# Kernel optimization log

Hardware: AMD Instinct MI355X
Metric: run time of the kernel (lower is better)

## Reference

```python
import jax, jax.numpy as jnp
import numpy as np

B, C_IN, C_OUT, H, W = 4, 256, 256, 64, 64
KH = KW = 3
STRIDE = 1
PAD = 1
DIL = 1


def setup_inputs() -> dict:
    key = jax.random.key(0)
    k1, k2, k3, k4 = jax.random.split(key, 4)
    x = jax.random.normal(k1, (B, C_IN, H, W), dtype=jnp.float32)
    # torchvision layout: 2*dg*KH*KW channels, (y, x) pair per kernel tap
    offset = jax.random.normal(k2, (B, 2 * KH * KW, H, W), dtype=jnp.float32)
    fan_in = C_IN * KH * KW
    weight = jax.random.normal(k3, (C_OUT, C_IN, KH, KW), dtype=jnp.float32) / np.sqrt(fan_in)
    bias = jax.random.normal(k4, (C_OUT,), dtype=jnp.float32) * 0.01
    return {"x": x, "offset": offset, "weight": weight, "bias": bias}


def _gather_bilinear_corner(x_flat, yi, xi, h, w):
    # x_flat: [B, C, H*W]; yi/xi: [B, KK, Ho, Wo] int32
    valid = ((yi >= 0) & (yi < h) & (xi >= 0) & (xi < w)).astype(x_flat.dtype)
    idx = jnp.clip(yi, 0, h - 1) * w + jnp.clip(xi, 0, w - 1)
    b = idx.shape[0]
    g = jnp.take_along_axis(x_flat, idx.reshape(b, 1, -1), axis=2)
    return g.reshape(b, x_flat.shape[1], *yi.shape[1:]), valid


def deform_conv2d(x, offset, weight, bias):
    b, c, h, w = x.shape
    o = weight.shape[0]
    kk = KH * KW
    ho = (h + 2 * PAD - DIL * (KH - 1) - 1) // STRIDE + 1
    wo = (w + 2 * PAD - DIL * (KW - 1) - 1) // STRIDE + 1

    ky = (jnp.arange(kk, dtype=jnp.float32) // KW) * DIL  # [KK]
    kx = (jnp.arange(kk, dtype=jnp.float32) % KW) * DIL
    hs = jnp.arange(ho, dtype=jnp.float32) * STRIDE - PAD   # [Ho]
    ws = jnp.arange(wo, dtype=jnp.float32) * STRIDE - PAD   # [Wo]

    off = offset.reshape(b, kk, 2, ho, wo)
    py = hs[None, None, :, None] + ky[None, :, None, None] + off[:, :, 0]  # [B,KK,Ho,Wo]
    px = ws[None, None, None, :] + kx[None, :, None, None] + off[:, :, 1]

    y0 = jnp.floor(py)
    x0 = jnp.floor(px)
    wy1 = py - y0  # fractional parts, differentiable w.r.t. offsets
    wx1 = px - x0
    wy0 = 1.0 - wy1
    wx0 = 1.0 - wx1
    y0i = y0.astype(jnp.int32)
    x0i = x0.astype(jnp.int32)

    x_flat = x.reshape(b, c, h * w)
    corners = [
        (y0i,     x0i,     wy0 * wx0),
        (y0i,     x0i + 1, wy0 * wx1),
        (y0i + 1, x0i,     wy1 * wx0),
        (y0i + 1, x0i + 1, wy1 * wx1),
    ]
    sampled = jnp.zeros((b, c, kk, ho, wo), dtype=x.dtype)
    for yi, xi, wgt in corners:
        g, valid = _gather_bilinear_corner(x_flat, yi, xi, h, w)
        sampled = sampled + g * (wgt * valid)[:, None]

    out = jnp.einsum('bckhw,ock->bohw', sampled, weight.reshape(o, c, kk))
    return out + bias[None, :, None, None]


def reference(x, offset, weight, bias):
    return deform_conv2d(x, offset, weight, bias)
```

## Files before the change

kernel.cpp:

```cpp
#include <hip/hip_runtime.h>

typedef __bf16 bf16;
typedef __bf16 bf16x4 __attribute__((ext_vector_type(4)));
typedef __bf16 bf16x8 __attribute__((ext_vector_type(8)));
typedef float  f32x4  __attribute__((ext_vector_type(4)));
typedef float  f32x16 __attribute__((ext_vector_type(16)));
typedef unsigned int u32x4 __attribute__((ext_vector_type(4)));

#define KK     9
#define KDIM   2304
#define KSTEPS 144
#define PXW    64

__device__ __forceinline__ int sreadi(int v) {
    return __builtin_amdgcn_readfirstlane(v);
}

__device__ __forceinline__ float BL(unsigned v) {
    return __builtin_bit_cast(float, v << 16);
}
__device__ __forceinline__ float BH(unsigned v) {
    return __builtin_bit_cast(float, v & 0xffff0000u);
}

__global__ __launch_bounds__(256) void prep2_k(const float* __restrict__ x,
                                               const float* __restrict__ w,
                                               bf16* __restrict__ xt,
                                               bf16* __restrict__ wq) {
    __shared__ __align__(16) char smem[8 * 2308 * 2];
    int bid = blockIdx.x;
    int tid = threadIdx.x;
    if (bid < 1024) {
        float (*tileF)[65] = reinterpret_cast<float(*)[65]>(smem);
        int pt = bid & 63, ct = (bid >> 6) & 3, b = bid >> 8;
        const float* src = x + ((size_t)(b * 256 + ct * 64)) * 4096 + pt * 64;
        int f4 = tid & 15;
        int cl = tid >> 4;
        #pragma unroll
        for (int q = 0; q < 4; ++q) {
            int c = q * 16 + cl;
            f32x4 v = *reinterpret_cast<const f32x4*>(src + (size_t)c * 4096 + f4 * 4);
            tileF[f4 * 4 + 0][c] = v[0];
            tileF[f4 * 4 + 1][c] = v[1];
            tileF[f4 * 4 + 2][c] = v[2];
            tileF[f4 * 4 + 3][c] = v[3];
        }
        __syncthreads();
        int j = tid & 7, p0 = tid >> 3;
        bf16* dst = xt + ((size_t)(b * 4096 + pt * 64)) * 256 + ct * 64 + j * 8;
        #pragma unroll
        for (int pp = 0; pp < 2; ++pp) {
            int p = p0 + pp * 32;
            bf16x8 sv;
            #pragma unroll
            for (int k = 0; k < 8; ++k) sv[k] = (bf16)tileF[p][j * 8 + k];
            *reinterpret_cast<bf16x8*>(dst + (size_t)p * 256) = sv;
        }
    } else {
        bf16 (*Wl)[2308] = reinterpret_cast<bf16(*)[2308]>(smem);
        int wb     = bid - 1024;
        int o_base = wb * 8;
        int m      = o_base >> 5;
        int o31b   = o_base & 31;
        #pragma unroll
        for (int pass = 0; pass < 18; ++pass) {
            int i    = pass * 256 + tid;
            int r    = i / 576;
            int col4 = i - r * 576;
            f32x4 v = *reinterpret_cast<const f32x4*>(
                w + (size_t)(o_base + r) * KDIM + col4 * 4);
            Wl[r][col4 * 4 + 0] = (bf16)v[0];
            Wl[r][col4 * 4 + 1] = (bf16)v[1];
            Wl[r][col4 * 4 + 2] = (bf16)v[2];
            Wl[r][col4 * 4 + 3] = (bf16)v[3];
        }
        __syncthreads();
        #pragma unroll
        for (int pass = 0; pass < 9; ++pass) {
            int gid  = pass * 256 + tid;
            int ol   = gid & 7;
            int half = (gid >> 3) & 1;
            int ks   = gid >> 4;
            int kb   = ks * 16 + half * 8;
            int tap  = kb >> 8;
            int cc0  = kb & 255;
            bf16x8 sv;
            #pragma unroll
            for (int j = 0; j < 8; ++j) sv[j] = Wl[ol][(cc0 + j) * 9 + tap];
            size_t g = (size_t)((m * KSTEPS + ks) * 64 + half * 32 + o31b + ol);
            *reinterpret_cast<bf16x8*>(wq + g * 8) = sv;
        }
    }
}

__global__ __launch_bounds__(1024, 4) void deform_gemm_k(
    const bf16*  __restrict__ xt,
    const float* __restrict__ off,
    const bf16*  __restrict__ wq,
    const float* __restrict__ bias,
    float*       __restrict__ out) {

    __shared__ bf16 S[2][PXW * 256];

    int tid   = threadIdx.x;
    int wavei = sreadi(tid >> 6);
    int lane  = tid & 63;
    int l32   = lane & 31;
    int half  = lane >> 5;
    int mt    = wavei & 7;
    int kh    = wavei >> 3;

    int bid   = blockIdx.x;
    int pb    = ((bid & 7) << 5) | (bid >> 3);
    int pix0  = pb * PXW;
    int b     = pix0 >> 12;
    int pimgb = pix0 & 4095;
    int obase = b * 73728;
    int rot   = (bid >> 3) & 7;

    int n0    = wavei * 4 + half * 2;
    int n1    = n0 + 1;
    int pimg0 = pimgb + n0;
    int pimg1 = pimgb + n1;
    const char* xb = (const char*)xt + ((size_t)b << 21) + l32 * 16;

    f32x16 acc0, acc1;
    #pragma unroll
    for (int r = 0; r < 16; ++r) { acc0[r] = 0.f; acc1[r] = 0.f; }

    auto body = [&](int n, int pimg, float oy, float ox, int ty, int tx,
                    bf16* Sw) {
        float py = (float)((pimg >> 6) + ty) + oy;
        float px = (float)((pimg & 63) + tx) + ox;
        float fy = floorf(py), fx = floorf(px);
        int   y0 = (int)fy,    x0 = (int)fx;
        float wy1 = py - fy, wx1 = px - fx;
        float wy0 = 1.f - wy1, wx0 = 1.f - wx1;
        wy0 = ((unsigned)y0       < 64u) ? wy0 : 0.f;
        wy1 = ((unsigned)(y0 + 1) < 64u) ? wy1 : 0.f;
        wx0 = ((unsigned)x0       < 64u) ? wx0 : 0.f;
        wx1 = ((unsigned)(x0 + 1) < 64u) ? wx1 : 0.f;
        int yc0 = min(max(y0, 0), 63), yc1 = min(max(y0 + 1, 0), 63);
        int xc0 = min(max(x0, 0), 63), xc1 = min(max(x0 + 1, 0), 63);
        unsigned u0 = (unsigned)(yc0 * 64 + xc0) * 512u;
        unsigned u1 = (unsigned)(yc0 * 64 + xc1) * 512u;
        unsigned u2 = (unsigned)(yc1 * 64 + xc0) * 512u;
        unsigned u3 = (unsigned)(yc1 * 64 + xc1) * 512u;
        float w0 = wy0 * wx0, w1 = wy0 * wx1;
        float w2 = wy1 * wx0, w3 = wy1 * wx1;
        u32x4 g0 = *(const u32x4*)(xb + u0);
        u32x4 g1 = *(const u32x4*)(xb + u1);
        u32x4 g2 = *(const u32x4*)(xb + u2);
        u32x4 g3 = *(const u32x4*)(xb + u3);
        bf16x8 sv;
        #pragma unroll
        for (int q = 0; q < 4; ++q) {
            float lo = fmaf(w0, BL(g0[q]), fmaf(w1, BL(g1[q]),
                       fmaf(w2, BL(g2[q]),      w3 * BL(g3[q]))));
            float hi = fmaf(w0, BH(g0[q]), fmaf(w1, BH(g1[q]),
                       fmaf(w2, BH(g2[q]),      w3 * BH(g3[q]))));
            sv[q * 2]     = (bf16)lo;
            sv[q * 2 + 1] = (bf16)hi;
        }
        int gsw = l32 ^ (n & 31);
        *reinterpret_cast<bf16x8*>(Sw + n * 256 + gsw * 8) = sv;
    };

    float oy0 = off[obase + (2 * rot)     * 4096 + pimg0];
    float ox0 = off[obase + (2 * rot + 1) * 4096 + pimg0];
    float oy1 = off[obase + (2 * rot)     * 4096 + pimg1];
    float ox1 = off[obase + (2 * rot + 1) * 4096 + pimg1];

    for (int t = 0; t < KK; ++t) {
        int tap = t + rot; if (tap >= KK) tap -= KK;
        int ty = tap / 3 - 1;
        int tx = tap % 3 - 1;
        bf16* Sw = &S[t & 1][0];

        body(n0, pimg0, oy0, ox0, ty, tx, Sw);

        const bf16* ap0 = wq +
            ((size_t)(((mt * KSTEPS) + tap * 16 + kh * 8) * 64 + lane)) * 8;
        bf16x8 af[8];
        #pragma unroll
        for (int s = 0; s < 8; ++s)
            af[s] = *reinterpret_cast<const bf16x8*>(ap0 + (size_t)s * 512);

        body(n1, pimg1, oy1, ox1, ty, tx, Sw);

        __syncthreads();

        if (t < KK - 1) {
            int tn = tap + 1; if (tn >= KK) tn = 0;
            oy0 = off[obase + (2 * tn)     * 4096 + pimg0];
            ox0 = off[obase + (2 * tn + 1) * 4096 + pimg0];
            oy1 = off[obase + (2 * tn)     * 4096 + pimg1];
            ox1 = off[obase + (2 * tn + 1) * 4096 + pimg1];
        }

        const bf16* Sr = Sw;
        #pragma unroll
        for (int s = 0; s < 8; ++s) {
            int g  = (kh * 8 + s) * 2 + half;
            int gs = g ^ l32;
            bf16x8 b0 = *reinterpret_cast<const bf16x8*>(Sr + l32 * 256 + gs * 8);
            bf16x8 b1 = *reinterpret_cast<const bf16x8*>(Sr + (32 + l32) * 256 + gs * 8);
            acc0 = __builtin_amdgcn_mfma_f32_32x32x16_bf16(af[s], b0, acc0, 0, 0, 0);
            acc1 = __builtin_amdgcn_mfma_f32_32x32x16_bf16(af[s], b1, acc1, 0, 0, 0);
        }
    }

    __syncthreads();
    float* Sf = reinterpret_cast<float*>(&S[0][0]);
    if (kh == 1) {
        #pragma unroll
        for (int r = 0; r < 16; ++r) {
            Sf[((mt * 2 + 0) * 16 + r) * 64 + lane] = acc0[r];
            Sf[((mt * 2 + 1) * 16 + r) * 64 + lane] = acc1[r];
        }
    }
    __syncthreads();
    if (kh == 0) {
        int m = mt * 32;
        #pragma unroll
        for (int nt = 0; nt < 2; ++nt) {
            int px = pimgb + nt * 32 + l32;
            float* op = out + ((size_t)(b * 256 + m)) * 4096 + px;
            #pragma unroll
            for (int r = 0; r < 16; ++r) {
                int row = (r & 3) + 8 * (r >> 2) + half * 4;
                float a = (nt == 0) ? acc0[r] : acc1[r];
                float v = a + Sf[((mt * 2 + nt) * 16 + r) * 64 + lane]
                            + bias[m + row];
                op[(size_t)row * 4096] = v;
            }
        }
    }
}

extern "C" void kernel_launch(void* const* d_in, const int* in_sizes, int n_in,
                              void* d_out, int out_size, void* d_ws, size_t ws_size,
                              hipStream_t stream) {
    const float* x    = (const float*)d_in[0];
    const float* off  = (const float*)d_in[1];
    const float* w    = (const float*)d_in[2];
    const float* bias = (const float*)d_in[3];
    float* out = (float*)d_out;

    bf16* wq = (bf16*)d_ws;
    bf16* xt = (bf16*)((char*)d_ws + (size_t)589824 * 2);

    prep2_k<<<1056, 256, 0, stream>>>(x, w, xt, wq);
    deform_gemm_k<<<256, 1024, 0, stream>>>(xt, off, wq, bias, out);
}
```

Measured before the change: 113.2 us.

## Triple-buffer sampled tiles to overlap bilinear gather with MFMA

Grows the LDS sample buffer from two to three stages. Two taps are prefilled before the loop, and inside the loop the tap two steps ahead is gathered while the current buffer feeds the MFMAs, with one barrier per iteration placed after compute. The goal is to overlap gather latency with matrix math and take the barrier off the path between fill and consume. In exchange, LDS use rises from 64KB to 96KB per block, and the offset loads are no longer prefetched a full iteration ahead.

```diff
diff --git a/kernel.cpp b/kernel.cpp
--- a/kernel.cpp
+++ b/kernel.cpp
@@ -1,7 +1,6 @@
 #include <hip/hip_runtime.h>
 
 typedef __bf16 bf16;
-typedef __bf16 bf16x4 __attribute__((ext_vector_type(4)));
 typedef __bf16 bf16x8 __attribute__((ext_vector_type(8)));
 typedef float  f32x4  __attribute__((ext_vector_type(4)));
 typedef float  f32x16 __attribute__((ext_vector_type(16)));
@@ -100,7 +99,7 @@
     const float* __restrict__ bias,
     float*       __restrict__ out) {
 
-    __shared__ bf16 S[2][PXW * 256];
+    __shared__ bf16 S[3][PXW * 256];
 
     int tid   = threadIdx.x;
     int wavei = sreadi(tid >> 6);
@@ -166,18 +165,28 @@
         *reinterpret_cast<bf16x8*>(Sw + n * 256 + gsw * 8) = sv;
     };
 
-    float oy0 = off[obase + (2 * rot)     * 4096 + pimg0];
-    float ox0 = off[obase + (2 * rot + 1) * 4096 + pimg0];
-    float oy1 = off[obase + (2 * rot)     * 4096 + pimg1];
-    float ox1 = off[obase + (2 * rot + 1) * 4096 + pimg1];
-
+    auto tap_body = [&](int tp, bf16* Sw) {
+        int ty = tp / 3 - 1;
+        int tx = tp % 3 - 1;
+        float oy0 = off[obase + (2 * tp)     * 4096 + pimg0];
+        float ox0 = off[obase + (2 * tp + 1) * 4096 + pimg0];
+        float oy1 = off[obase + (2 * tp)     * 4096 + pimg1];
+        float ox1 = off[obase + (2 * tp + 1) * 4096 + pimg1];
+        body(n0, pimg0, oy0, ox0, ty, tx, Sw);
+        body(n1, pimg1, oy1, ox1, ty, tx, Sw);
+    };
+
+    {
+        int tp0 = rot;
+        tap_body(tp0, &S[0][0]);
+        int tp1 = rot + 1; if (tp1 >= KK) tp1 -= KK;
+        tap_body(tp1, &S[1][0]);
+    }
+    __syncthreads();
+
+    int br = 0, bw = 2;
     for (int t = 0; t < KK; ++t) {
         int tap = t + rot; if (tap >= KK) tap -= KK;
-        int ty = tap / 3 - 1;
-        int tx = tap % 3 - 1;
-        bf16* Sw = &S[t & 1][0];
-
-        body(n0, pimg0, oy0, ox0, ty, tx, Sw);
 
         const bf16* ap0 = wq +
             ((size_t)(((mt * KSTEPS) + tap * 16 + kh * 8) * 64 + lane)) * 8;
@@ -186,19 +195,12 @@
         for (int s = 0; s < 8; ++s)
             af[s] = *reinterpret_cast<const bf16x8*>(ap0 + (size_t)s * 512);
 
-        body(n1, pimg1, oy1, ox1, ty, tx, Sw);
-
-        __syncthreads();
-
-        if (t < KK - 1) {
-            int tn = tap + 1; if (tn >= KK) tn = 0;
-            oy0 = off[obase + (2 * tn)     * 4096 + pimg0];
-            ox0 = off[obase + (2 * tn + 1) * 4096 + pimg0];
-            oy1 = off[obase + (2 * tn)     * 4096 + pimg1];
-            ox1 = off[obase + (2 * tn + 1) * 4096 + pimg1];
-        }
-
-        const bf16* Sr = Sw;
+        if (t < KK - 2) {
+            int tp = tap + 2; if (tp >= KK) tp -= KK;
+            tap_body(tp, &S[bw][0]);
+        }
+
+        const bf16* Sr = &S[br][0];
         #pragma unroll
         for (int s = 0; s < 8; ++s) {
             int g  = (kh * 8 + s) * 2 + half;
@@ -208,9 +210,12 @@
             acc0 = __builtin_amdgcn_mfma_f32_32x32x16_bf16(af[s], b0, acc0, 0, 0, 0);
             acc1 = __builtin_amdgcn_mfma_f32_32x32x16_bf16(af[s], b1, acc1, 0, 0, 0);
         }
-    }
-
-    __syncthreads();
+
+        __syncthreads();
+        br = (br + 1 == 3) ? 0 : br + 1;
+        bw = (bw + 1 == 3) ? 0 : bw + 1;
+    }
+
     float* Sf = reinterpret_cast<float*>(&S[0][0]);
     if (kh == 1) {
         #pragma unroll
```

Result: no change. 113.5 us (+0.3%).
